# Optimization experiments

Hardware: AMD Instinct MI355X
Metric: run time of the kernel (lower is better)

Reference implementation:

```python
import jax, jax.numpy as jnp
import numpy as np

B, T, F, H, R, K = 256, 512, 128, 128, 8, 64
LAG_IDX = 0


def setup_inputs() -> dict:
    key = jax.random.key(0)
    ks = jax.random.split(key, 14)
    s_ih = 1.0 / np.sqrt(F)
    s_hh = 1.0 / np.sqrt(H)
    return {
        "x": jax.random.normal(ks[0], (B, T, F), jnp.float32),
        "regime": jax.random.randint(ks[1], (B, T), 0, R, jnp.int32),
        "lag_scale": jnp.asarray(0.9, jnp.float32),
        "lag_bias": jnp.asarray(0.0, jnp.float32),
        "Wih0": jax.random.normal(ks[2], (3 * H, F), jnp.float32) * s_ih,
        "Whh0": jax.random.normal(ks[3], (3 * H, H), jnp.float32) * s_hh,
        "bih0": jax.random.normal(ks[4], (3 * H,), jnp.float32) * s_hh,
        "bhh0": jax.random.normal(ks[5], (3 * H,), jnp.float32) * s_hh,
        "Wih1": jax.random.normal(ks[6], (3 * H, H), jnp.float32) * s_hh,
        "Whh1": jax.random.normal(ks[7], (3 * H, H), jnp.float32) * s_hh,
        "bih1": jax.random.normal(ks[8], (3 * H,), jnp.float32) * s_hh,
        "bhh1": jax.random.normal(ks[9], (3 * H,), jnp.float32) * s_hh,
        "W1": jax.random.normal(ks[10], (R, H, K), jnp.float32) * s_hh,
        "b1": jax.random.normal(ks[11], (R, K), jnp.float32) * 0.1,
        "W2": jax.random.normal(ks[12], (R, K), jnp.float32) * 0.05,
        "b2": jax.random.normal(ks[13], (R,), jnp.float32) * 0.05,
    }


def _gru_layer(x_tbf, Wih, Whh, bih, bhh):
    # PyTorch GRU cell, gate order (r, z, n). x_tbf: (T, B, Fin)
    Hh = Whh.shape[1]

    def step(h, xt):
        gi = xt @ Wih.T + bih            # (B, 3H)
        gh = h @ Whh.T + bhh             # (B, 3H)
        ir, iz, inn = jnp.split(gi, 3, axis=-1)
        hr, hz, hn = jnp.split(gh, 3, axis=-1)
        r = jax.nn.sigmoid(ir + hr)
        z = jax.nn.sigmoid(iz + hz)
        n = jnp.tanh(inn + r * hn)
        h_new = (1.0 - z) * n + z * h
        return h_new, h_new

    h0 = jnp.zeros((x_tbf.shape[1], Hh), x_tbf.dtype)
    _, ys = jax.lax.scan(step, h0, x_tbf)
    return ys                             # (T, B, H)


def reference(x, regime, lag_scale, lag_bias,
              Wih0, Whh0, bih0, bhh0,
              Wih1, Whh1, bih1, bhh1,
              W1, b1, W2, b2):
    lag_pred = lag_scale * x[:, :, LAG_IDX] + lag_bias          # (B, T)

    xt = jnp.transpose(x, (1, 0, 2))                            # (T, B, F)
    h1 = _gru_layer(xt, Wih0, Whh0, bih0, bhh0)
    h2 = _gru_layer(h1, Wih1, Whh1, bih1, bhh1)
    out = jnp.transpose(h2, (1, 0, 2))                          # (B, T, H)

    Bq, Tq, Hq = out.shape
    out_flat = out.reshape(-1, Hq)                              # (N, H)
    reg = regime.reshape(-1)                                    # (N,)

    # regime-specific heads: Linear(H,64) -> SiLU -> Linear(64,1)
    a = jnp.einsum('nh,rhk->nrk', out_flat, W1) + b1            # (N, R, K)
    a = jnp.take_along_axis(a, reg[:, None, None].astype(jnp.int32), axis=1)[:, 0, :]
    a = a * jax.nn.sigmoid(a)                                   # SiLU
    corr = jnp.einsum('nk,nk->n', a, W2[reg]) + b2[reg]         # (N,)

    return lag_pred + corr.reshape(Bq, Tq)
```

## Files before the change

kernel.cpp:

```cpp
#include <hip/hip_runtime.h>
#include <hip/hip_bf16.h>
#include <cstdint>

#define B_ 256
#define T_ 512
#define F_ 128
#define H_ 128
#define G3_ 384
#define R_ 8
#define K_ 64

typedef __attribute__((ext_vector_type(8))) short short8_t;
typedef __attribute__((ext_vector_type(4))) float f32x4;
typedef __attribute__((ext_vector_type(2))) float f32x2;

__device__ __forceinline__ float sigm(float x) { return 1.f / (1.f + __expf(-x)); }
__device__ __forceinline__ float tanh_f(float x) { return 1.f - 2.f / (1.f + __expf(2.f * x)); }
__device__ __forceinline__ unsigned short f2bf(float f) {
    uint32_t u = __builtin_bit_cast(uint32_t, f);
    return (unsigned short)((u + 0x7FFFu + ((u >> 16) & 1u)) >> 16);
}
__device__ __forceinline__ short8_t pack8(float4 a, float4 b) {
    short8_t v;
    v[0] = (short)f2bf(a.x); v[1] = (short)f2bf(a.y);
    v[2] = (short)f2bf(a.z); v[3] = (short)f2bf(a.w);
    v[4] = (short)f2bf(b.x); v[5] = (short)f2bf(b.y);
    v[6] = (short)f2bf(b.z); v[7] = (short)f2bf(b.w);
    return v;
}

__device__ __forceinline__ float dpp_red2(float x) {
    int a = __builtin_amdgcn_mov_dpp(__builtin_bit_cast(int, x), 0xB1, 0xF, 0xF, true);
    x += __builtin_bit_cast(float, a);
    int b = __builtin_amdgcn_mov_dpp(__builtin_bit_cast(int, x), 0x4E, 0xF, 0xF, true);
    x += __builtin_bit_cast(float, b);
    return x;
}

__global__ __launch_bounds__(512, 2) void gemm_gi_mfma(const float* __restrict__ A,
                                                       const float* __restrict__ W,
                                                       const float* __restrict__ bias,
                                                       float* __restrict__ C)
{
    __shared__ alignas(16) unsigned short A_lds[128 * 128];

    const int tid = threadIdx.x;
    const int wv = tid >> 6, lane = tid & 63;
    const int lc = lane & 15, lg = lane >> 4;
    const size_t m0 = (size_t)blockIdx.x * 128;

    short8_t bf[3][4];
    float bi[3];
    #pragma unroll
    for (int u = 0; u < 3; ++u) {
        const int n = 48 * wv + 16 * u + lc;
        bi[u] = bias[n];
        #pragma unroll
        for (int ks = 0; ks < 4; ++ks) {
            const float4* wp = (const float4*)(W + (size_t)n * 128 + ks * 32 + lg * 8);
            bf[u][ks] = pack8(wp[0], wp[1]);
        }
    }

    {
        const int m = tid >> 2, kq = tid & 3;
        const float4* ap = (const float4*)(A + (m0 + m) * 128 + kq * 32);
        float4 v0 = ap[0], v1 = ap[1], v2 = ap[2], v3 = ap[3];
        float4 v4 = ap[4], v5 = ap[5], v6 = ap[6], v7 = ap[7];
        char* base = (char*)A_lds;
        const int bb = m * 256 + kq * 64, sw = (m & 7) << 4;
        *(short8_t*)(base + ((bb +  0) ^ sw)) = pack8(v0, v1);
        *(short8_t*)(base + ((bb + 16) ^ sw)) = pack8(v2, v3);
        *(short8_t*)(base + ((bb + 32) ^ sw)) = pack8(v4, v5);
        *(short8_t*)(base + ((bb + 48) ^ sw)) = pack8(v6, v7);
    }
    __syncthreads();

    const char* Ab = (const char*)A_lds;
    #pragma unroll 2
    for (int mt = 0; mt < 8; ++mt) {
        short8_t af0 = *(const short8_t*)(Ab + (((mt * 16 + lc) * 256 +  0 + lg * 16) ^ ((lc & 7) << 4)));
        short8_t af1 = *(const short8_t*)(Ab + (((mt * 16 + lc) * 256 + 64 + lg * 16) ^ ((lc & 7) << 4)));
        short8_t af2 = *(const short8_t*)(Ab + (((mt * 16 + lc) * 256 + 128 + lg * 16) ^ ((lc & 7) << 4)));
        short8_t af3 = *(const short8_t*)(Ab + (((mt * 16 + lc) * 256 + 192 + lg * 16) ^ ((lc & 7) << 4)));
        f32x4 a0 = {0.f, 0.f, 0.f, 0.f}, a1 = a0, a2 = a0;
        a0 = __builtin_amdgcn_mfma_f32_16x16x32_bf16(af0, bf[0][0], a0, 0, 0, 0);
        a1 = __builtin_amdgcn_mfma_f32_16x16x32_bf16(af0, bf[1][0], a1, 0, 0, 0);
        a2 = __builtin_amdgcn_mfma_f32_16x16x32_bf16(af0, bf[2][0], a2, 0, 0, 0);
        a0 = __builtin_amdgcn_mfma_f32_16x16x32_bf16(af1, bf[0][1], a0, 0, 0, 0);
        a1 = __builtin_amdgcn_mfma_f32_16x16x32_bf16(af1, bf[1][1], a1, 0, 0, 0);
        a2 = __builtin_amdgcn_mfma_f32_16x16x32_bf16(af1, bf[2][1], a2, 0, 0, 0);
        a0 = __builtin_amdgcn_mfma_f32_16x16x32_bf16(af2, bf[0][2], a0, 0, 0, 0);
        a1 = __builtin_amdgcn_mfma_f32_16x16x32_bf16(af2, bf[1][2], a1, 0, 0, 0);
        a2 = __builtin_amdgcn_mfma_f32_16x16x32_bf16(af2, bf[2][2], a2, 0, 0, 0);
        a0 = __builtin_amdgcn_mfma_f32_16x16x32_bf16(af3, bf[0][3], a0, 0, 0, 0);
        a1 = __builtin_amdgcn_mfma_f32_16x16x32_bf16(af3, bf[1][3], a1, 0, 0, 0);
        a2 = __builtin_amdgcn_mfma_f32_16x16x32_bf16(af3, bf[2][3], a2, 0, 0, 0);
        #pragma unroll
        for (int r = 0; r < 4; ++r) {
            float* cp = C + (m0 + mt * 16 + 4 * lg + r) * G3_ + 48 * wv + lc;
            cp[0]  = a0[r] + bi[0];
            cp[16] = a1[r] + bi[1];
            cp[32] = a2[r] + bi[2];
        }
    }
}

__global__ __launch_bounds__(512, 1) void gru_seq(const float* __restrict__ gi,
                                                  const float* __restrict__ Whh,
                                                  const float* __restrict__ bhh,
                                                  float* __restrict__ hout)
{
    __shared__ alignas(16) float hbuf[2][4][36];

    const int tid = threadIdx.x;
    const int b = blockIdx.x;
    const int w = tid >> 6, lane = tid & 63;
    const int j = 16 * w + (lane >> 2);
    const int s = lane & 3;
    const bool fin = (s == 0);

    f32x2 wr2[16], wz2[16], wn2[16];
    {
        const float4* p0 = (const float4*)(Whh + (size_t)j * 128 + s * 32);
        const float4* p1 = (const float4*)(Whh + (size_t)(128 + j) * 128 + s * 32);
        const float4* p2 = (const float4*)(Whh + (size_t)(256 + j) * 128 + s * 32);
        #pragma unroll
        for (int q = 0; q < 8; ++q) {
            float4 v0 = p0[q], v1 = p1[q], v2 = p2[q];
            wr2[2*q]   = f32x2{v0.x, v0.y};
            wr2[2*q+1] = f32x2{v0.z, v0.w};
            wz2[2*q]   = f32x2{v1.x, v1.y};
            wz2[2*q+1] = f32x2{v1.z, v1.w};
            wn2[2*q]   = f32x2{v2.x, v2.y};
            wn2[2*q+1] = f32x2{v2.z, v2.w};
        }
    }
    const float br = bhh[j], bz = bhh[128 + j], bn = bhh[256 + j];

    if (tid < H_) hbuf[0][tid >> 5][tid & 31] = 0.f;
    __syncthreads();

    const float* gip = gi + (size_t)b * T_ * G3_ + j;
    float* hop = hout + (size_t)b * T_ * H_ + j;

    float g0[3], g1[3], g2[3], g3[3];
    if (fin) {
        #pragma unroll
        for (int u = 0; u < 3; ++u) {
            g0[u] = gip[0 * G3_ + 128 * u];
            g1[u] = gip[1 * G3_ + 128 * u];
            g2[u] = gip[2 * G3_ + 128 * u];
            g3[u] = gip[3 * G3_ + 128 * u];
        }
    }
    float hprev = 0.f;

    auto step = [&](int t, float (&gc)[3]) {
        const int p = t & 1;
        const float4* hv = (const float4*)(&hbuf[p][s][0]);
        f32x2 pr2 = {0.f, 0.f}, pz2 = pr2, pn2 = pr2;
        #pragma unroll
        for (int q = 0; q < 8; ++q) {
            float4 h4 = hv[q];
            f32x2 ha = {h4.x, h4.y};
            f32x2 hb = {h4.z, h4.w};
            pr2 += wr2[2*q] * ha;  pr2 += wr2[2*q+1] * hb;
            pz2 += wz2[2*q] * ha;  pz2 += wz2[2*q+1] * hb;
            pn2 += wn2[2*q] * ha;  pn2 += wn2[2*q+1] * hb;
        }
        float pr = dpp_red2(pr2[0] + pr2[1]);
        float pz = dpp_red2(pz2[0] + pz2[1]);
        float pn = dpp_red2(pn2[0] + pn2[1]);

        if (fin) {
            float r  = sigm(gc[0] + pr + br);
            float z  = sigm(gc[1] + pz + bz);
            float nn = tanh_f(gc[2] + r * (pn + bn));
            float h  = (1.f - z) * nn + z * hprev;
            hprev = h;
            hbuf[p ^ 1][j >> 5][j & 31] = h;
            hop[(size_t)t * H_] = h;
            int tn = (t + 4 < T_) ? t + 4 : T_ - 1;
            const float* gp = gip + (size_t)tn * G3_;
            gc[0] = gp[0]; gc[1] = gp[128]; gc[2] = gp[256];
        }
        asm volatile("s_waitcnt lgkmcnt(0)" ::: "memory");
        __builtin_amdgcn_s_barrier();
    };

    for (int t = 0; t < T_; t += 4) {
        step(t + 0, g0);
        step(t + 1, g1);
        step(t + 2, g2);
        step(t + 3, g3);
    }
}

__global__ __launch_bounds__(256) void head_k(const float* __restrict__ h2,
                                              const float* __restrict__ x,
                                              const int* __restrict__ regime,
                                              const float* __restrict__ W1,
                                              const float* __restrict__ b1,
                                              const float* __restrict__ W2,
                                              const float* __restrict__ b2,
                                              const float* __restrict__ lag_scale,
                                              const float* __restrict__ lag_bias,
                                              float* __restrict__ out)
{
    __shared__ alignas(16) float hrow[4][128];
    const int tid = threadIdx.x;
    const int wv = tid >> 6, lane = tid & 63;
    const size_t s = (size_t)blockIdx.x * 4 + wv;
    const int reg = regime[s];

    if (lane < 32)
        ((float4*)hrow[wv])[lane] = ((const float4*)(h2 + s * H_))[lane];
    __syncthreads();

    float acc = b1[reg * K_ + lane];
    const float* Wp = W1 + (size_t)reg * H_ * K_ + lane;
    const float4* h4p = (const float4*)hrow[wv];
    #pragma unroll
    for (int q = 0; q < 32; ++q) {
        float4 h4 = h4p[q];
        acc += h4.x * Wp[(4 * q + 0) * K_];
        acc += h4.y * Wp[(4 * q + 1) * K_];
        acc += h4.z * Wp[(4 * q + 2) * K_];
        acc += h4.w * Wp[(4 * q + 3) * K_];
    }
    float silu = acc * sigm(acc);
    float v = silu * W2[reg * K_ + lane];
    #pragma unroll
    for (int m = 1; m < 64; m <<= 1) v += __shfl_xor(v, m);
    if (lane == 0) {
        float lag = lag_scale[0] * x[s * F_] + lag_bias[0];
        out[s] = lag + v + b2[reg];
    }
}

extern "C" void kernel_launch(void* const* d_in, const int* in_sizes, int n_in,
                              void* d_out, int out_size, void* d_ws, size_t ws_size,
                              hipStream_t stream) {
    const float* x         = (const float*)d_in[0];
    const int*   regime    = (const int*)d_in[1];
    const float* lag_scale = (const float*)d_in[2];
    const float* lag_bias  = (const float*)d_in[3];
    const float* Wih0      = (const float*)d_in[4];
    const float* Whh0      = (const float*)d_in[5];
    const float* bih0      = (const float*)d_in[6];
    const float* bhh0      = (const float*)d_in[7];
    const float* Wih1      = (const float*)d_in[8];
    const float* Whh1      = (const float*)d_in[9];
    const float* bih1      = (const float*)d_in[10];
    const float* bhh1      = (const float*)d_in[11];
    const float* W1        = (const float*)d_in[12];
    const float* b1        = (const float*)d_in[13];
    const float* W2        = (const float*)d_in[14];
    const float* b2        = (const float*)d_in[15];
    float* out = (float*)d_out;

    const size_t NT = (size_t)B_ * T_;
    const size_t need = NT * G3_ * 4 + NT * H_ * 4;
    if (ws_size < need) {
        hipMemsetAsync(d_out, 0x7F, (size_t)out_size * 4, stream);
        return;
    }
    float* gi = (float*)d_ws;
    float* hb = gi + NT * G3_;

    const int gblocks = (int)(NT / 128);
    gemm_gi_mfma<<<gblocks, 512, 0, stream>>>(x, Wih0, bih0, gi);
    gru_seq<<<B_, 512, 0, stream>>>(gi, Whh0, bhh0, hb);
    gemm_gi_mfma<<<gblocks, 512, 0, stream>>>(hb, Wih1, bih1, gi);
    gru_seq<<<B_, 512, 0, stream>>>(gi, Whh1, bhh1, hb);
    head_k<<<(int)(NT / 4), 256, 0, stream>>>(hb, x, regime, W1, b1, W2, b2,
                                              lag_scale, lag_bias, out);
}
```

Measured before the change: 955.3 us.

## Store GRU input projections as gate-interleaved bf16 for single-load fetch

The input-projection GEMM now writes its output as bf16, interleaving the r/z/n gates per hidden unit into a padded 4-slot layout staged through LDS for coalesced 16-byte stores. The recurrent kernel then fetches all three gate preactivations for a step with one 8-byte load instead of three scattered fp32 loads, halving workspace traffic. The GRU kernel's launch bounds are raised to allow two blocks per CU. The cost is bf16 rounding of the gate inputs, plus extra barriers and LDS staging in the GEMM.

```diff
diff --git a/kernel.cpp b/kernel.cpp
--- a/kernel.cpp
+++ b/kernel.cpp
@@ -13,6 +13,8 @@
 typedef __attribute__((ext_vector_type(8))) short short8_t;
 typedef __attribute__((ext_vector_type(4))) float f32x4;
 typedef __attribute__((ext_vector_type(2))) float f32x2;
+typedef __attribute__((ext_vector_type(4))) unsigned int u32x4;
+typedef __attribute__((ext_vector_type(2))) unsigned int u32x2;
 
 __device__ __forceinline__ float sigm(float x) { return 1.f / (1.f + __expf(-x)); }
 __device__ __forceinline__ float tanh_f(float x) { return 1.f - 2.f / (1.f + __expf(2.f * x)); }
@@ -40,9 +42,10 @@
 __global__ __launch_bounds__(512, 2) void gemm_gi_mfma(const float* __restrict__ A,
                                                        const float* __restrict__ W,
                                                        const float* __restrict__ bias,
-                                                       float* __restrict__ C)
+                                                       unsigned short* __restrict__ C)
 {
     __shared__ alignas(16) unsigned short A_lds[128 * 128];
+    __shared__ alignas(16) unsigned short D_lds[16 * 520];
 
     const int tid = threadIdx.x;
     const int wv = tid >> 6, lane = tid & 63;
@@ -51,9 +54,14 @@
 
     short8_t bf[3][4];
     float bi[3];
+    int col[3];
+    bool zpad[3];
     #pragma unroll
     for (int u = 0; u < 3; ++u) {
         const int n = 48 * wv + 16 * u + lc;
+        const int g = n >> 7, j = n & 127;
+        col[u] = j * 4 + g;
+        zpad[u] = (g == 0);
         bi[u] = bias[n];
         #pragma unroll
         for (int ks = 0; ks < 4; ++ks) {
@@ -77,7 +85,6 @@
     __syncthreads();
 
     const char* Ab = (const char*)A_lds;
-    #pragma unroll 2
     for (int mt = 0; mt < 8; ++mt) {
         short8_t af0 = *(const short8_t*)(Ab + (((mt * 16 + lc) * 256 +  0 + lg * 16) ^ ((lc & 7) << 4)));
         short8_t af1 = *(const short8_t*)(Ab + (((mt * 16 + lc) * 256 + 64 + lg * 16) ^ ((lc & 7) << 4)));
@@ -96,17 +103,34 @@
         a0 = __builtin_amdgcn_mfma_f32_16x16x32_bf16(af3, bf[0][3], a0, 0, 0, 0);
         a1 = __builtin_amdgcn_mfma_f32_16x16x32_bf16(af3, bf[1][3], a1, 0, 0, 0);
         a2 = __builtin_amdgcn_mfma_f32_16x16x32_bf16(af3, bf[2][3], a2, 0, 0, 0);
+
+        asm volatile("s_waitcnt lgkmcnt(0)" ::: "memory");
+        __builtin_amdgcn_s_barrier();
         #pragma unroll
         for (int r = 0; r < 4; ++r) {
-            float* cp = C + (m0 + mt * 16 + 4 * lg + r) * G3_ + 48 * wv + lc;
-            cp[0]  = a0[r] + bi[0];
-            cp[16] = a1[r] + bi[1];
-            cp[32] = a2[r] + bi[2];
-        }
-    }
-}
-
-__global__ __launch_bounds__(512, 1) void gru_seq(const float* __restrict__ gi,
+            unsigned short* row = D_lds + (4 * lg + r) * 520;
+            row[col[0]] = f2bf(a0[r] + bi[0]);
+            row[col[1]] = f2bf(a1[r] + bi[1]);
+            row[col[2]] = f2bf(a2[r] + bi[2]);
+            if (zpad[0]) row[col[0] + 3] = 0;
+            if (zpad[1]) row[col[1] + 3] = 0;
+            if (zpad[2]) row[col[2] + 3] = 0;
+        }
+        asm volatile("s_waitcnt lgkmcnt(0)" ::: "memory");
+        __builtin_amdgcn_s_barrier();
+
+        u32x4* cg = (u32x4*)(C + (m0 + mt * 16) * 512);
+        #pragma unroll
+        for (int i = 0; i < 2; ++i) {
+            int idx = tid + 512 * i;
+            int row = idx >> 6, un = idx & 63;
+            const u32x4* src = (const u32x4*)(D_lds + row * 520 + un * 8);
+            cg[idx] = *src;
+        }
+    }
+}
+
+__global__ __launch_bounds__(512, 2) void gru_seq(const unsigned short* __restrict__ gi,
                                                   const float* __restrict__ Whh,
                                                   const float* __restrict__ bhh,
                                                   float* __restrict__ hout)
@@ -141,22 +165,19 @@
     if (tid < H_) hbuf[0][tid >> 5][tid & 31] = 0.f;
     __syncthreads();
 
-    const float* gip = gi + (size_t)b * T_ * G3_ + j;
+    const char* gipb = (const char*)gi + (size_t)b * T_ * 1024 + (size_t)j * 8;
     float* hop = hout + (size_t)b * T_ * H_ + j;
 
-    float g0[3], g1[3], g2[3], g3[3];
+    u32x2 g0 = {0,0}, g1 = g0, g2 = g0, g3 = g0;
     if (fin) {
-        #pragma unroll
-        for (int u = 0; u < 3; ++u) {
-            g0[u] = gip[0 * G3_ + 128 * u];
-            g1[u] = gip[1 * G3_ + 128 * u];
-            g2[u] = gip[2 * G3_ + 128 * u];
-            g3[u] = gip[3 * G3_ + 128 * u];
-        }
+        g0 = *(const u32x2*)(gipb + 0 * 1024);
+        g1 = *(const u32x2*)(gipb + 1 * 1024);
+        g2 = *(const u32x2*)(gipb + 2 * 1024);
+        g3 = *(const u32x2*)(gipb + 3 * 1024);
     }
     float hprev = 0.f;
 
-    auto step = [&](int t, float (&gc)[3]) {
+    auto step = [&](int t, u32x2& gc) {
         const int p = t & 1;
         const float4* hv = (const float4*)(&hbuf[p][s][0]);
         f32x2 pr2 = {0.f, 0.f}, pz2 = pr2, pn2 = pr2;
@@ -174,16 +195,18 @@
         float pn = dpp_red2(pn2[0] + pn2[1]);
 
         if (fin) {
-            float r  = sigm(gc[0] + pr + br);
-            float z  = sigm(gc[1] + pz + bz);
-            float nn = tanh_f(gc[2] + r * (pn + bn));
+            float gr = __builtin_bit_cast(float, gc[0] << 16);
+            float gz = __builtin_bit_cast(float, gc[0] & 0xFFFF0000u);
+            float gn = __builtin_bit_cast(float, gc[1] << 16);
+            float r  = sigm(gr + pr + br);
+            float z  = sigm(gz + pz + bz);
+            float nn = tanh_f(gn + r * (pn + bn));
             float h  = (1.f - z) * nn + z * hprev;
             hprev = h;
             hbuf[p ^ 1][j >> 5][j & 31] = h;
             hop[(size_t)t * H_] = h;
             int tn = (t + 4 < T_) ? t + 4 : T_ - 1;
-            const float* gp = gip + (size_t)tn * G3_;
-            gc[0] = gp[0]; gc[1] = gp[128]; gc[2] = gp[256];
+            gc = *(const u32x2*)(gipb + (size_t)tn * 1024);
         }
         asm volatile("s_waitcnt lgkmcnt(0)" ::: "memory");
         __builtin_amdgcn_s_barrier();
@@ -261,13 +284,13 @@
     float* out = (float*)d_out;
 
     const size_t NT = (size_t)B_ * T_;
-    const size_t need = NT * G3_ * 4 + NT * H_ * 4;
+    const size_t need = NT * 512 * 2 + NT * H_ * 4;
     if (ws_size < need) {
         hipMemsetAsync(d_out, 0x7F, (size_t)out_size * 4, stream);
         return;
     }
-    float* gi = (float*)d_ws;
-    float* hb = gi + NT * G3_;
+    unsigned short* gi = (unsigned short*)d_ws;
+    float* hb = (float*)(gi + NT * 512);
 
     const int gblocks = (int)(NT / 128);
     gemm_gi_mfma<<<gblocks, 512, 0, stream>>>(x, Wih0, bih0, gi);
```

Measured after the change: 875.6 us. 8.3% less time.
